# Kernel tuning notes

Hardware: AMD Instinct MI355X
Metric: run time of the kernel (lower is better)

## Reference

```python
import jax, jax.numpy as jnp
import numpy as np

C = 128   # c_pair
N = 512   # num residues (pair grid side)
OUTGOING = True
EPS = 1e-5


def _layernorm(x, w, b):
    m = jnp.mean(x, axis=-1, keepdims=True)
    v = jnp.var(x, axis=-1, keepdims=True)
    return (x - m) * jax.lax.rsqrt(v + EPS) * w + b


def setup_inputs() -> dict:
    key = jax.random.key(0)
    ks = jax.random.split(key, 8)
    s = 1.0 / np.sqrt(C)
    return {
        "act": jax.random.normal(ks[0], (N, N, C), jnp.float32),
        "mask": (jax.random.uniform(ks[1], (N, N)) > 0.1).astype(jnp.float32),
        "ln_in_w": jnp.ones((C,), jnp.float32),
        "ln_in_b": jnp.zeros((C,), jnp.float32),
        "W_proj": jax.random.normal(ks[2], (2 * C, C), jnp.float32) * s,
        "W_gate": jax.random.normal(ks[3], (2 * C, C), jnp.float32) * s,
        "ln_c_w": jnp.ones((C,), jnp.float32),
        "ln_c_b": jnp.zeros((C,), jnp.float32),
        "W_out": jax.random.normal(ks[4], (C, C), jnp.float32) * s,
        "W_glin": jax.random.normal(ks[5], (C, C), jnp.float32) * s,
    }


def reference(act, mask, ln_in_w, ln_in_b, W_proj, W_gate, ln_c_w, ln_c_b, W_out, W_glin):
    # left input layernorm
    x = _layernorm(act, ln_in_w, ln_in_b)                       # [N,N,C]
    # masked, sigmoid-gated projection to 2C channels
    p = jnp.einsum('ijc,dc->ijd', x, W_proj)                    # [N,N,2C]
    p = p * mask[..., None]
    p = p * jax.nn.sigmoid(jnp.einsum('ijc,dc->ijd', x, W_gate))
    a, b = p[..., :C], p[..., C:]
    # triangle einsum (channel-first 'cik,cjk->cij' or 'ckj,cki->cij',
    # written channel-last here)
    if OUTGOING:
        t = jnp.einsum('ikc,jkc->ijc', a, b)                    # [N,N,C]
    else:
        t = jnp.einsum('kjc,kic->ijc', a, b)
    # center norm + output projection, gated by sigmoid of normalized input
    t = _layernorm(t, ln_c_w, ln_c_b)
    out = jnp.einsum('ijc,dc->ijd', t, W_out)
    out = out * jax.nn.sigmoid(jnp.einsum('ijc,dc->ijd', x, W_glin))
    return out
```

## Files before the change

### kernel.cpp

```cpp
#include <hip/hip_runtime.h>


#define NN 512
#define CC 128
#define NPOS (NN * NN)
#define LN_EPS 1e-5f

typedef __attribute__((ext_vector_type(8))) short bf16x8;
typedef __attribute__((ext_vector_type(4))) float f32x4;

__device__ __forceinline__ float bitf(unsigned int u) {
    return __builtin_bit_cast(float, u);
}
__device__ __forceinline__ float b2f(unsigned short u) {
    return bitf(((unsigned int)u) << 16);
}
__device__ __forceinline__ unsigned short f2b(float f) {
    unsigned int u = __builtin_bit_cast(unsigned int, f);
    u = u + 0x7FFFu + ((u >> 16) & 1u);
    return (unsigned short)(u >> 16);
}
__device__ __forceinline__ float sigmoidf(float x) {
    return 1.0f / (1.0f + __expf(-x));
}
__device__ __forceinline__ void unpack8(uint4 u, float* dst) {
    dst[0] = bitf(u.x << 16); dst[1] = bitf(u.x & 0xFFFF0000u);
    dst[2] = bitf(u.y << 16); dst[3] = bitf(u.y & 0xFFFF0000u);
    dst[4] = bitf(u.z << 16); dst[5] = bitf(u.z & 0xFFFF0000u);
    dst[6] = bitf(u.w << 16); dst[7] = bitf(u.w & 0xFFFF0000u);
}

__global__ __launch_bounds__(256) void k_ln_proj(
    const float* __restrict__ act, const float* __restrict__ mask,
    const float* __restrict__ lw, const float* __restrict__ lb,
    const float* __restrict__ Wproj, const float* __restrict__ Wgate,
    const float* __restrict__ Wglin,
    unsigned short* __restrict__ a_ws, unsigned short* __restrict__ b_ws,
    unsigned short* __restrict__ g_ws)
{
    __shared__ __align__(16) unsigned short Xs[128 * 136];
    __shared__ __align__(16) float WL[4352];
    unsigned short* Wu = (unsigned short*)WL;

    const int tid = threadIdx.x;
    const int m0 = blockIdx.x * 128;

    {
        const int c4 = tid & 31;
        float4 w4 = *(const float4*)(lw + c4 * 4);
        float4 b4 = *(const float4*)(lb + c4 * 4);
        for (int it = 0; it < 16; ++it) {
            int p = (tid >> 5) + it * 8;
            float4 v = *(const float4*)(act + (size_t)(m0 + p) * CC + c4 * 4);
            float s  = v.x + v.y + v.z + v.w;
            float ss = v.x * v.x + v.y * v.y + v.z * v.z + v.w * v.w;
            #pragma unroll
            for (int ofs = 1; ofs < 32; ofs <<= 1) {
                s  += __shfl_xor(s, ofs);
                ss += __shfl_xor(ss, ofs);
            }
            float mean = s * (1.0f / 128.0f);
            float var  = ss * (1.0f / 128.0f) - mean * mean;
            float rstd = rsqrtf(var + LN_EPS);
            ushort4 o;
            o.x = f2b((v.x - mean) * rstd * w4.x + b4.x);
            o.y = f2b((v.y - mean) * rstd * w4.y + b4.y);
            o.z = f2b((v.z - mean) * rstd * w4.z + b4.z);
            o.w = f2b((v.w - mean) * rstd * w4.w + b4.w);
            *(ushort4*)&Xs[p * 136 + c4 * 4] = o;
        }
    }

    const int lane  = tid & 63;
    const int wid   = tid >> 6;
    const int row16 = lane & 15, kg = lane >> 4;
    const int wrm = (wid >> 1) * 64;
    const int wcn = (wid & 1) * 32;

    for (int chunk = 0; chunk < 10; ++chunk) {
        __syncthreads();
        {
            int r = tid >> 2, q = tid & 3;
            const float* wrow;
            if (chunk < 8) {
                int d = chunk * 32 + (r >> 1);
                wrow = (r & 1) ? (Wgate + d * CC) : (Wproj + d * CC);
            } else {
                wrow = Wglin + ((chunk - 8) * 64 + r) * CC;
            }
            #pragma unroll
            for (int t = 0; t < 8; ++t) {
                float4 v = *(const float4*)(wrow + q * 32 + t * 4);
                ushort4 o;
                o.x = f2b(v.x); o.y = f2b(v.y); o.z = f2b(v.z); o.w = f2b(v.w);
                *(ushort4*)&Wu[r * 136 + q * 32 + t * 4] = o;
            }
        }
        __syncthreads();

        f32x4 acc[4][2] = {};
        #pragma unroll
        for (int ks = 0; ks < 4; ++ks) {
            const int koff = ks * 32 + kg * 8;
            bf16x8 xa[4], wb[2];
            #pragma unroll
            for (int mf = 0; mf < 4; ++mf)
                xa[mf] = *(const bf16x8*)&Xs[(wrm + mf * 16 + row16) * 136 + koff];
            #pragma unroll
            for (int nf = 0; nf < 2; ++nf)
                wb[nf] = *(const bf16x8*)&Wu[(wcn + nf * 16 + row16) * 136 + koff];
            #pragma unroll
            for (int mf = 0; mf < 4; ++mf)
                #pragma unroll
                for (int nf = 0; nf < 2; ++nf)
                    acc[mf][nf] = __builtin_amdgcn_mfma_f32_16x16x32_bf16(
                        xa[mf], wb[nf], acc[mf][nf], 0, 0, 0);
        }

        for (int h = 0; h < 2; ++h) {
            __syncthreads();
            if ((wid >> 1) == h) {
                #pragma unroll
                for (int nf = 0; nf < 2; ++nf) {
                    #pragma unroll
                    for (int mf = 0; mf < 4; ++mf) {
                        int r = wcn + nf * 16 + row16;
                        int mloc = mf * 16 + kg * 4;
                        float* dst = &WL[r * 66 + mloc];
                        f32x4 v = acc[mf][nf];
                        *(float2*)(dst)     = make_float2(v.x, v.y);
                        *(float2*)(dst + 2) = make_float2(v.z, v.w);
                    }
                }
            }
            __syncthreads();
            if (chunk < 8) {
                int dd = tid >> 3, mseg = tid & 7;
                float4 p0 = *(const float4*)&WL[(2 * dd) * 66 + mseg * 8];
                float4 p1 = *(const float4*)&WL[(2 * dd) * 66 + mseg * 8 + 4];
                float4 g0 = *(const float4*)&WL[(2 * dd + 1) * 66 + mseg * 8];
                float4 g1 = *(const float4*)&WL[(2 * dd + 1) * 66 + mseg * 8 + 4];
                const float* mkp = mask + m0 + h * 64 + mseg * 8;
                float4 mk0 = *(const float4*)(mkp);
                float4 mk1 = *(const float4*)(mkp + 4);
                unsigned short ob[8];
                ob[0] = f2b(p0.x * mk0.x * sigmoidf(g0.x));
                ob[1] = f2b(p0.y * mk0.y * sigmoidf(g0.y));
                ob[2] = f2b(p0.z * mk0.z * sigmoidf(g0.z));
                ob[3] = f2b(p0.w * mk0.w * sigmoidf(g0.w));
                ob[4] = f2b(p1.x * mk1.x * sigmoidf(g1.x));
                ob[5] = f2b(p1.y * mk1.y * sigmoidf(g1.y));
                ob[6] = f2b(p1.z * mk1.z * sigmoidf(g1.z));
                ob[7] = f2b(p1.w * mk1.w * sigmoidf(g1.w));
                unsigned short* plane = (chunk < 4) ? a_ws : b_ws;
                int D = (chunk & 3) * 32 + dd;
                uint4 w;
                w.x = (unsigned)ob[0] | ((unsigned)ob[1] << 16);
                w.y = (unsigned)ob[2] | ((unsigned)ob[3] << 16);
                w.z = (unsigned)ob[4] | ((unsigned)ob[5] << 16);
                w.w = (unsigned)ob[6] | ((unsigned)ob[7] << 16);
                *(uint4*)(plane + (size_t)D * NPOS + m0 + h * 64 + mseg * 8) = w;
            } else {
                int mm = tid >> 2, q = tid & 3;
                unsigned short ob[16];
                #pragma unroll
                for (int rr = 0; rr < 16; ++rr)
                    ob[rr] = f2b(sigmoidf(WL[(q * 16 + rr) * 66 + mm]));
                uint4 w0, w1;
                w0.x = (unsigned)ob[0]  | ((unsigned)ob[1]  << 16);
                w0.y = (unsigned)ob[2]  | ((unsigned)ob[3]  << 16);
                w0.z = (unsigned)ob[4]  | ((unsigned)ob[5]  << 16);
                w0.w = (unsigned)ob[6]  | ((unsigned)ob[7]  << 16);
                w1.x = (unsigned)ob[8]  | ((unsigned)ob[9]  << 16);
                w1.y = (unsigned)ob[10] | ((unsigned)ob[11] << 16);
                w1.z = (unsigned)ob[12] | ((unsigned)ob[13] << 16);
                w1.w = (unsigned)ob[14] | ((unsigned)ob[15] << 16);
                unsigned short* gp = g_ws + (size_t)(m0 + h * 64 + mm) * CC +
                                     (chunk - 8) * 64 + q * 16;
                *(uint4*)gp = w0;
                *(uint4*)(gp + 8) = w1;
            }
        }
    }
}

__global__ __launch_bounds__(256) void k_tri(
    const unsigned short* __restrict__ a_ws,
    const unsigned short* __restrict__ b_ws,
    unsigned short* __restrict__ t_ws)
{
    __shared__ __align__(16) unsigned short As[8192];
    __shared__ __align__(16) unsigned short Bs[8192];

    const int tid  = threadIdx.x;
    const int lane = tid & 63;
    const int wid  = tid >> 6;
    const int c    = blockIdx.y;
    const int i0   = (blockIdx.x >> 2) * 128;
    const int j0   = (blockIdx.x & 3) * 128;

    const size_t plane = (size_t)c * NPOS;
    const unsigned short* Ag = a_ws + plane + (size_t)i0 * NN;
    const unsigned short* Bg = b_ws + plane + (size_t)j0 * NN;

    const int row16 = lane & 15, kg = lane >> 4;
    const int wrm = (wid >> 1) * 64;
    const int wcn = (wid & 1) * 64;
    const int xr  = (lane & 7) << 4;

    int srcOff[4];
    #pragma unroll
    for (int q = 0; q < 4; ++q) {
        int p  = (wid * 4 + q) * 1024 + lane * 16;
        int lg = p ^ (((p >> 7) & 7) << 4);
        int r = lg >> 7, k16 = (lg >> 4) & 7;
        srcOff[q] = r * NN + k16 * 8;
    }

    f32x4 acc[4][4] = {};

    for (int kt = 0; kt < 8; ++kt) {
        const int k0 = kt * 64;
        __syncthreads();
        #pragma unroll
        for (int q = 0; q < 4; ++q) {
            int ldsOff = (wid * 4 + q) * 512;
            __builtin_amdgcn_global_load_lds(
                (const __attribute__((address_space(1))) void*)(Ag + srcOff[q] + k0),
                (__attribute__((address_space(3))) void*)(As + ldsOff), 16, 0, 0);
            __builtin_amdgcn_global_load_lds(
                (const __attribute__((address_space(1))) void*)(Bg + srcOff[q] + k0),
                (__attribute__((address_space(3))) void*)(Bs + ldsOff), 16, 0, 0);
        }
        __syncthreads();

        #pragma unroll
        for (int ks = 0; ks < 2; ++ks) {
            const int kb = ks * 64 + kg * 16;
            bf16x8 af[4], bfr[4];
            #pragma unroll
            for (int mf = 0; mf < 4; ++mf) {
                int lA = ((wrm + mf * 16 + row16) << 7) + kb;
                af[mf] = *(const bf16x8*)((const char*)As + (lA ^ xr));
            }
            #pragma unroll
            for (int nf = 0; nf < 4; ++nf) {
                int lB = ((wcn + nf * 16 + row16) << 7) + kb;
                bfr[nf] = *(const bf16x8*)((const char*)Bs + (lB ^ xr));
            }
            #pragma unroll
            for (int mf = 0; mf < 4; ++mf)
                #pragma unroll
                for (int nf = 0; nf < 4; ++nf)
                    acc[mf][nf] = __builtin_amdgcn_mfma_f32_16x16x32_bf16(
                        af[mf], bfr[nf], acc[mf][nf], 0, 0, 0);
        }
    }

    unsigned short* tp = t_ws + plane;
    #pragma unroll
    for (int mf = 0; mf < 4; ++mf) {
        int i = i0 + wrm + mf * 16 + kg * 4;
        #pragma unroll
        for (int nf = 0; nf < 4; ++nf) {
            int j = j0 + wcn + nf * 16 + row16;
            f32x4 v = acc[mf][nf];
            tp[(size_t)(i + 0) * NN + j] = f2b(v.x);
            tp[(size_t)(i + 1) * NN + j] = f2b(v.y);
            tp[(size_t)(i + 2) * NN + j] = f2b(v.z);
            tp[(size_t)(i + 3) * NN + j] = f2b(v.w);
        }
    }
}

__global__ __launch_bounds__(256) void k_out(
    const unsigned short* __restrict__ tT,
    const unsigned short* __restrict__ g_ws,
    const float* __restrict__ lw, const float* __restrict__ lb,
    const float* __restrict__ Wout,
    float* __restrict__ out)
{
    __shared__ __align__(16) float Xf[128 * 68];
    __shared__ __align__(16) unsigned short Wt[128 * 132];

    const int tid = threadIdx.x;
    const int m0 = blockIdx.x * 64;

    #pragma unroll
    for (int it = 0; it < 4; ++it) {
        int c  = (tid >> 3) + it * 32;
        int mg = tid & 7;
        uint4 u = *(const uint4*)(tT + (size_t)c * NPOS + m0 + mg * 8);
        float f[8];
        unpack8(u, f);
        float* dst = &Xf[c * 68 + mg * 8];
        #pragma unroll
        for (int t = 0; t < 8; ++t) dst[t] = f[t];
    }
    #pragma unroll
    for (int it = 0; it < 16; ++it) {
        int idx = tid + it * 256;
        int d = idx >> 5, c4 = idx & 31;
        float4 v = *(const float4*)(Wout + d * CC + c4 * 4);
        Wt[(c4 * 4 + 0) * 132 + d] = f2b(v.x);
        Wt[(c4 * 4 + 1) * 132 + d] = f2b(v.y);
        Wt[(c4 * 4 + 2) * 132 + d] = f2b(v.z);
        Wt[(c4 * 4 + 3) * 132 + d] = f2b(v.w);
    }
    __syncthreads();

    {
        int m = tid >> 2, q = tid & 3;
        float s = 0.f, ss = 0.f;
        #pragma unroll
        for (int t = 0; t < 32; ++t) {
            float v = Xf[(q * 32 + t) * 68 + m];
            s += v; ss += v * v;
        }
        s += __shfl_xor(s, 1); ss += __shfl_xor(ss, 1);
        s += __shfl_xor(s, 2); ss += __shfl_xor(ss, 2);
        float mean = s * (1.0f / 128.0f);
        float var  = ss * (1.0f / 128.0f) - mean * mean;
        float rstd = rsqrtf(var + LN_EPS);
        #pragma unroll
        for (int t = 0; t < 32; ++t) {
            int c = q * 32 + t;
            float v = Xf[c * 68 + m];
            Xf[c * 68 + m] = (v - mean) * rstd * lw[c] + lb[c];
        }
    }
    __syncthreads();

    const int tx = tid & 15, ty = tid >> 4;
    float acc[4][8] = {};
    #pragma unroll 4
    for (int c = 0; c < 128; ++c) {
        float4 xv = *(const float4*)&Xf[c * 68 + ty * 4];
        const unsigned short* wp = &Wt[c * 132 + tx * 8];
        uint2 wa = *(const uint2*)(wp);
        uint2 wbu = *(const uint2*)(wp + 4);
        float w[8];
        w[0] = bitf(wa.x << 16);  w[1] = bitf(wa.x & 0xFFFF0000u);
        w[2] = bitf(wa.y << 16);  w[3] = bitf(wa.y & 0xFFFF0000u);
        w[4] = bitf(wbu.x << 16); w[5] = bitf(wbu.x & 0xFFFF0000u);
        w[6] = bitf(wbu.y << 16); w[7] = bitf(wbu.y & 0xFFFF0000u);
        float xr[4] = {xv.x, xv.y, xv.z, xv.w};
        #pragma unroll
        for (int i2 = 0; i2 < 4; ++i2)
            #pragma unroll
            for (int j = 0; j < 8; ++j)
                acc[i2][j] += xr[i2] * w[j];
    }

    #pragma unroll
    for (int i2 = 0; i2 < 4; ++i2) {
        int m = m0 + ty * 4 + i2;
        const unsigned short* gp = g_ws + (size_t)m * CC + tx * 8;
        ushort4 ga = *(const ushort4*)(gp);
        ushort4 gb = *(const ushort4*)(gp + 4);
        float4 o0, o1;
        o0.x = acc[i2][0] * b2f(ga.x);
        o0.y = acc[i2][1] * b2f(ga.y);
        o0.z = acc[i2][2] * b2f(ga.z);
        o0.w = acc[i2][3] * b2f(ga.w);
        o1.x = acc[i2][4] * b2f(gb.x);
        o1.y = acc[i2][5] * b2f(gb.y);
        o1.z = acc[i2][6] * b2f(gb.z);
        o1.w = acc[i2][7] * b2f(gb.w);
        *(float4*)(out + (size_t)m * CC + tx * 8) = o0;
        *(float4*)(out + (size_t)m * CC + tx * 8 + 4) = o1;
    }
}

extern "C" void kernel_launch(void* const* d_in, const int* in_sizes, int n_in,
                              void* d_out, int out_size, void* d_ws, size_t ws_size,
                              hipStream_t stream) {
    const float* act   = (const float*)d_in[0];
    const float* mask  = (const float*)d_in[1];
    const float* lnw   = (const float*)d_in[2];
    const float* lnb   = (const float*)d_in[3];
    const float* Wproj = (const float*)d_in[4];
    const float* Wgate = (const float*)d_in[5];
    const float* lncw  = (const float*)d_in[6];
    const float* lncb  = (const float*)d_in[7];
    const float* Wout  = (const float*)d_in[8];
    const float* Wglin = (const float*)d_in[9];
    float* out = (float*)d_out;

    char* ws = (char*)d_ws;
    unsigned short* a_ws = (unsigned short*)(ws);
    unsigned short* b_ws = (unsigned short*)(ws + 67108864);
    unsigned short* g_ws = (unsigned short*)(ws + 134217728);
    unsigned short* t_ws = (unsigned short*)(ws + 201326592);

    k_ln_proj<<<dim3(2048), dim3(256), 0, stream>>>(
        act, mask, lnw, lnb, Wproj, Wgate, Wglin, a_ws, b_ws, g_ws);

    k_tri<<<dim3(16, 128), dim3(256), 0, stream>>>(a_ws, b_ws, t_ws);

    k_out<<<dim3(4096), dim3(256), 0, stream>>>(
        t_ws, g_ws, lncw, lncb, Wout, out);
}
```

Baseline: 607.3 us.

## Pre-convert weights to swizzled bf16, direct-to-LDS loads, register epilogue, XCD-aware tri grid

A small pre-kernel converts the projection and gate weights to bf16 once, in a swizzled layout stored in the t workspace. The projection kernel then loads them straight into LDS with global_load_lds, replacing the per-block fp32 load and convert. The projection epilogue no longer stages results through LDS with extra barriers. It pairs proj and gate values with lane shuffles and writes directly from registers, at the cost of narrower, scattered stores for the g output. The triangle kernel's grid is remapped so that all tiles of a channel land on the same XCD, to improve L2 reuse.

```diff
diff --git a/kernel.cpp b/kernel.cpp
--- a/kernel.cpp
+++ b/kernel.cpp
@@ -30,17 +30,45 @@
     dst[6] = bitf(u.w << 16); dst[7] = bitf(u.w & 0xFFFF0000u);
 }
 
+__global__ __launch_bounds__(256) void k_wprep(
+    const float* __restrict__ Wproj, const float* __restrict__ Wgate,
+    const float* __restrict__ Wglin, unsigned short* __restrict__ Wpb)
+{
+    const int chunk = blockIdx.x;
+    const int tid = threadIdx.x;
+    #pragma unroll
+    for (int j = 0; j < 4; ++j) {
+        int u = tid * 4 + j;
+        int p = u * 16;
+        int l = p ^ (((p >> 8) & 7) << 4);
+        int r = l >> 8;
+        int k0 = (l & 255) >> 1;
+        const float* src;
+        if (chunk < 8) {
+            int d = chunk * 32 + (r >> 1);
+            src = (r & 1) ? (Wgate + d * CC) : (Wproj + d * CC);
+        } else {
+            src = Wglin + ((chunk - 8) * 64 + r) * CC;
+        }
+        float4 v0 = *(const float4*)(src + k0);
+        float4 v1 = *(const float4*)(src + k0 + 4);
+        ushort4 o0, o1;
+        o0.x = f2b(v0.x); o0.y = f2b(v0.y); o0.z = f2b(v0.z); o0.w = f2b(v0.w);
+        o1.x = f2b(v1.x); o1.y = f2b(v1.y); o1.z = f2b(v1.z); o1.w = f2b(v1.w);
+        *(ushort4*)(Wpb + chunk * 8192 + u * 8)     = o0;
+        *(ushort4*)(Wpb + chunk * 8192 + u * 8 + 4) = o1;
+    }
+}
+
 __global__ __launch_bounds__(256) void k_ln_proj(
     const float* __restrict__ act, const float* __restrict__ mask,
     const float* __restrict__ lw, const float* __restrict__ lb,
-    const float* __restrict__ Wproj, const float* __restrict__ Wgate,
-    const float* __restrict__ Wglin,
+    const unsigned short* __restrict__ Wpb,
     unsigned short* __restrict__ a_ws, unsigned short* __restrict__ b_ws,
     unsigned short* __restrict__ g_ws)
 {
     __shared__ __align__(16) unsigned short Xs[128 * 136];
-    __shared__ __align__(16) float WL[4352];
-    unsigned short* Wu = (unsigned short*)WL;
+    __shared__ __align__(16) unsigned short Wu[8192];
 
     const int tid = threadIdx.x;
     const int m0 = blockIdx.x * 128;
@@ -76,25 +104,21 @@
     const int row16 = lane & 15, kg = lane >> 4;
     const int wrm = (wid >> 1) * 64;
     const int wcn = (wid & 1) * 32;
+    const int xrW = (row16 & 7) << 4;
+
+    float4 mk4[4];
+    #pragma unroll
+    for (int mf = 0; mf < 4; ++mf)
+        mk4[mf] = *(const float4*)(mask + m0 + wrm + mf * 16 + kg * 4);
 
     for (int chunk = 0; chunk < 10; ++chunk) {
         __syncthreads();
-        {
-            int r = tid >> 2, q = tid & 3;
-            const float* wrow;
-            if (chunk < 8) {
-                int d = chunk * 32 + (r >> 1);
-                wrow = (r & 1) ? (Wgate + d * CC) : (Wproj + d * CC);
-            } else {
-                wrow = Wglin + ((chunk - 8) * 64 + r) * CC;
-            }
-            #pragma unroll
-            for (int t = 0; t < 8; ++t) {
-                float4 v = *(const float4*)(wrow + q * 32 + t * 4);
-                ushort4 o;
-                o.x = f2b(v.x); o.y = f2b(v.y); o.z = f2b(v.z); o.w = f2b(v.w);
-                *(ushort4*)&Wu[r * 136 + q * 32 + t * 4] = o;
-            }
+        #pragma unroll
+        for (int q = 0; q < 4; ++q) {
+            int off = (wid * 4 + q) * 512 + lane * 8;
+            __builtin_amdgcn_global_load_lds(
+                (const __attribute__((address_space(1))) void*)(Wpb + chunk * 8192 + off),
+                (__attribute__((address_space(3))) void*)(Wu + off), 16, 0, 0);
         }
         __syncthreads();
 
@@ -107,8 +131,10 @@
             for (int mf = 0; mf < 4; ++mf)
                 xa[mf] = *(const bf16x8*)&Xs[(wrm + mf * 16 + row16) * 136 + koff];
             #pragma unroll
-            for (int nf = 0; nf < 2; ++nf)
-                wb[nf] = *(const bf16x8*)&Wu[(wcn + nf * 16 + row16) * 136 + koff];
+            for (int nf = 0; nf < 2; ++nf) {
+                int pb = (((wcn + nf * 16 + row16) << 8) + (koff << 1)) ^ xrW;
+                wb[nf] = *(const bf16x8*)((const char*)Wu + pb);
+            }
             #pragma unroll
             for (int mf = 0; mf < 4; ++mf)
                 #pragma unroll
@@ -117,68 +143,43 @@
                         xa[mf], wb[nf], acc[mf][nf], 0, 0, 0);
         }
 
-        for (int h = 0; h < 2; ++h) {
-            __syncthreads();
-            if ((wid >> 1) == h) {
+        if (chunk < 8) {
+            unsigned short* plane = (chunk < 4) ? a_ws : b_ws;
+            #pragma unroll
+            for (int mf = 0; mf < 4; ++mf) {
                 #pragma unroll
                 for (int nf = 0; nf < 2; ++nf) {
-                    #pragma unroll
-                    for (int mf = 0; mf < 4; ++mf) {
-                        int r = wcn + nf * 16 + row16;
-                        int mloc = mf * 16 + kg * 4;
-                        float* dst = &WL[r * 66 + mloc];
-                        f32x4 v = acc[mf][nf];
-                        *(float2*)(dst)     = make_float2(v.x, v.y);
-                        *(float2*)(dst + 2) = make_float2(v.z, v.w);
+                    f32x4 p = acc[mf][nf];
+                    float gx = __shfl_xor(p.x, 1);
+                    float gy = __shfl_xor(p.y, 1);
+                    float gz = __shfl_xor(p.z, 1);
+                    float gw = __shfl_xor(p.w, 1);
+                    if (!(row16 & 1)) {
+                        int rn = wcn + nf * 16 + row16;
+                        int D = (chunk * 32 + (rn >> 1)) & 127;
+                        ushort4 o;
+                        o.x = f2b(p.x * mk4[mf].x * sigmoidf(gx));
+                        o.y = f2b(p.y * mk4[mf].y * sigmoidf(gy));
+                        o.z = f2b(p.z * mk4[mf].z * sigmoidf(gz));
+                        o.w = f2b(p.w * mk4[mf].w * sigmoidf(gw));
+                        *(ushort4*)(plane + (size_t)D * NPOS +
+                                    m0 + wrm + mf * 16 + kg * 4) = o;
                     }
                 }
             }
-            __syncthreads();
-            if (chunk < 8) {
-                int dd = tid >> 3, mseg = tid & 7;
-                float4 p0 = *(const float4*)&WL[(2 * dd) * 66 + mseg * 8];
-                float4 p1 = *(const float4*)&WL[(2 * dd) * 66 + mseg * 8 + 4];
-                float4 g0 = *(const float4*)&WL[(2 * dd + 1) * 66 + mseg * 8];
-                float4 g1 = *(const float4*)&WL[(2 * dd + 1) * 66 + mseg * 8 + 4];
-                const float* mkp = mask + m0 + h * 64 + mseg * 8;
-                float4 mk0 = *(const float4*)(mkp);
-                float4 mk1 = *(const float4*)(mkp + 4);
-                unsigned short ob[8];
-                ob[0] = f2b(p0.x * mk0.x * sigmoidf(g0.x));
-                ob[1] = f2b(p0.y * mk0.y * sigmoidf(g0.y));
-                ob[2] = f2b(p0.z * mk0.z * sigmoidf(g0.z));
-                ob[3] = f2b(p0.w * mk0.w * sigmoidf(g0.w));
-                ob[4] = f2b(p1.x * mk1.x * sigmoidf(g1.x));
-                ob[5] = f2b(p1.y * mk1.y * sigmoidf(g1.y));
-                ob[6] = f2b(p1.z * mk1.z * sigmoidf(g1.z));
-                ob[7] = f2b(p1.w * mk1.w * sigmoidf(g1.w));
-                unsigned short* plane = (chunk < 4) ? a_ws : b_ws;
-                int D = (chunk & 3) * 32 + dd;
-                uint4 w;
-                w.x = (unsigned)ob[0] | ((unsigned)ob[1] << 16);
-                w.y = (unsigned)ob[2] | ((unsigned)ob[3] << 16);
-                w.z = (unsigned)ob[4] | ((unsigned)ob[5] << 16);
-                w.w = (unsigned)ob[6] | ((unsigned)ob[7] << 16);
-                *(uint4*)(plane + (size_t)D * NPOS + m0 + h * 64 + mseg * 8) = w;
-            } else {
-                int mm = tid >> 2, q = tid & 3;
-                unsigned short ob[16];
+        } else {
+            #pragma unroll
+            for (int mf = 0; mf < 4; ++mf) {
+                int mb = m0 + wrm + mf * 16 + kg * 4;
                 #pragma unroll
-                for (int rr = 0; rr < 16; ++rr)
-                    ob[rr] = f2b(sigmoidf(WL[(q * 16 + rr) * 66 + mm]));
-                uint4 w0, w1;
-                w0.x = (unsigned)ob[0]  | ((unsigned)ob[1]  << 16);
-                w0.y = (unsigned)ob[2]  | ((unsigned)ob[3]  << 16);
-                w0.z = (unsigned)ob[4]  | ((unsigned)ob[5]  << 16);
-                w0.w = (unsigned)ob[6]  | ((unsigned)ob[7]  << 16);
-                w1.x = (unsigned)ob[8]  | ((unsigned)ob[9]  << 16);
-                w1.y = (unsigned)ob[10] | ((unsigned)ob[11] << 16);
-                w1.z = (unsigned)ob[12] | ((unsigned)ob[13] << 16);
-                w1.w = (unsigned)ob[14] | ((unsigned)ob[15] << 16);
-                unsigned short* gp = g_ws + (size_t)(m0 + h * 64 + mm) * CC +
-                                     (chunk - 8) * 64 + q * 16;
-                *(uint4*)gp = w0;
-                *(uint4*)(gp + 8) = w1;
+                for (int nf = 0; nf < 2; ++nf) {
+                    int d = (chunk - 8) * 64 + wcn + nf * 16 + row16;
+                    f32x4 p = acc[mf][nf];
+                    g_ws[(size_t)(mb + 0) * CC + d] = f2b(sigmoidf(p.x));
+                    g_ws[(size_t)(mb + 1) * CC + d] = f2b(sigmoidf(p.y));
+                    g_ws[(size_t)(mb + 2) * CC + d] = f2b(sigmoidf(p.z));
+                    g_ws[(size_t)(mb + 3) * CC + d] = f2b(sigmoidf(p.w));
+                }
             }
         }
     }
@@ -195,9 +196,14 @@
     const int tid  = threadIdx.x;
     const int lane = tid & 63;
     const int wid  = tid >> 6;
-    const int c    = blockIdx.y;
-    const int i0   = (blockIdx.x >> 2) * 128;
-    const int j0   = (blockIdx.x & 3) * 128;
+
+    const int virt = blockIdx.x;
+    const int xcd  = virt & 7;
+    const int idx  = virt >> 3;
+    const int c    = xcd * 16 + (idx >> 4);
+    const int tile = idx & 15;
+    const int i0   = (tile >> 2) * 128;
+    const int j0   = (tile & 3) * 128;
 
     const size_t plane = (size_t)c * NPOS;
     const unsigned short* Ag = a_ws + plane + (size_t)i0 * NN;
@@ -392,11 +398,14 @@
     unsigned short* b_ws = (unsigned short*)(ws + 67108864);
     unsigned short* g_ws = (unsigned short*)(ws + 134217728);
     unsigned short* t_ws = (unsigned short*)(ws + 201326592);
+    unsigned short* Wpb  = t_ws;
+
+    k_wprep<<<dim3(10), dim3(256), 0, stream>>>(Wproj, Wgate, Wglin, Wpb);
 
     k_ln_proj<<<dim3(2048), dim3(256), 0, stream>>>(
-        act, mask, lnw, lnb, Wproj, Wgate, Wglin, a_ws, b_ws, g_ws);
-
-    k_tri<<<dim3(16, 128), dim3(256), 0, stream>>>(a_ws, b_ws, t_ws);
+        act, mask, lnw, lnb, Wpb, a_ws, b_ws, g_ws);
+
+    k_tri<<<dim3(2048), dim3(256), 0, stream>>>(a_ws, b_ws, t_ws);
 
     k_out<<<dim3(4096), dim3(256), 0, stream>>>(
         t_ws, g_ws, lncw, lncb, Wout, out);
```

Measured after the change: 566.2 us. 1.07x faster.
